# Kernel tuning notes

Hardware: AMD Instinct MI355X
Metric: run time of the kernel (lower is better)

The kernel has to match this reference:

```python
import jax, jax.numpy as jnp
import numpy as np

EMBED = 512
HEADS = 8
HEAD_DIM = EMBED // HEADS
EPS = 1e-5


def setup_inputs() -> dict:
    key = jax.random.key(0)
    ks = jax.random.split(key, 10)
    s = 1.0 / np.sqrt(EMBED)
    x = jax.random.normal(ks[0], (2, 4096, EMBED), dtype=jnp.float32)
    Wq = jax.random.uniform(ks[1], (EMBED, EMBED), jnp.float32, -s, s)
    bq = jnp.zeros((EMBED,), jnp.float32)
    Wk = jax.random.uniform(ks[2], (EMBED, EMBED), jnp.float32, -s, s)
    bk = jnp.zeros((EMBED,), jnp.float32)
    Wv = jax.random.uniform(ks[3], (EMBED, EMBED), jnp.float32, -s, s)
    bv = jnp.zeros((EMBED,), jnp.float32)
    Wo = jax.random.uniform(ks[4], (EMBED, EMBED), jnp.float32, -s, s)
    bo = jnp.zeros((EMBED,), jnp.float32)
    gamma = jnp.ones((EMBED,), jnp.float32)
    beta = jnp.zeros((EMBED,), jnp.float32)
    return {"x": x, "Wq": Wq, "bq": bq, "Wk": Wk, "bk": bk,
            "Wv": Wv, "bv": bv, "Wo": Wo, "bo": bo,
            "gamma": gamma, "beta": beta}


def reference(x, Wq, bq, Wk, bk, Wv, bv, Wo, bo, gamma, beta):
    b, n, e = x.shape
    def split_heads(t):  # [b,n,e] -> [b,h,n,d]
        return t.reshape(b, n, HEADS, HEAD_DIM).transpose(0, 2, 1, 3)
    q = split_heads(x @ Wq + bq)
    k = split_heads(x @ Wk + bk)
    v = split_heads(x @ Wv + bv)
    energy = jnp.einsum('bhqd,bhkd->bhqk', q, k) * (HEAD_DIM ** -0.5)
    attn = jax.nn.softmax(energy, axis=-1)  # dropout=0.0 (eval)
    out = jnp.einsum('bhqk,bhkd->bhqd', attn, v)
    out = out.transpose(0, 2, 1, 3).reshape(b, n, e)
    out = out @ Wo + bo
    y = x + out
    mu = jnp.mean(y, axis=-1, keepdims=True)
    var = jnp.var(y, axis=-1, keepdims=True)
    return (y - mu) * jax.lax.rsqrt(var + EPS) * gamma + beta
```

## Files before the change

### kernel.cpp

```cpp
#include <hip/hip_runtime.h>
#include <hip/hip_bf16.h>


#define ROWS 8192
#define EMB  512
#define SEQ  4096
#define HEADS 8
#define HD   64
#define QSCALE 0.18033688011112042f

typedef __attribute__((ext_vector_type(8))) short bf16x8;
typedef __attribute__((ext_vector_type(4))) short bf16x4;
typedef __attribute__((ext_vector_type(4))) float f32x4;

#define MFMA_K16(A, B, C) __builtin_amdgcn_mfma_f32_16x16x16bf16_1k(A, B, C, 0, 0, 0)

__device__ __forceinline__ float bf16_to_f(unsigned short u) {
    union { unsigned int i; float f; } v; v.i = ((unsigned int)u) << 16; return v.f;
}
__device__ __forceinline__ unsigned short f_to_bf16(float f) {
    union { __hip_bfloat16 h; unsigned short u; } v; v.h = __float2bfloat16(f); return v.u;
}
__device__ __forceinline__ unsigned int pack_bf16_trunc(float a, float b) {
    return __builtin_amdgcn_perm(__float_as_uint(b), __float_as_uint(a), 0x07060302u);
}
__device__ __forceinline__ void load_lds16(const void* g, void* l) {
    __builtin_amdgcn_global_load_lds(
        (const __attribute__((address_space(1))) void*)g,
        (__attribute__((address_space(3))) void*)l, 16, 0, 0);
}

__global__ void detect_kernel(const void* x, int* flag) {
    const unsigned short* p = (const unsigned short*)x;
    int t = threadIdx.x;
    int cnt = 0;
    for (int i = 0; i < 4; ++i) {
        unsigned short u = p[t * 4 + i];
        int e = (u >> 7) & 0xFF;
        if (e >= 140) cnt++;
    }
    for (int off = 32; off > 0; off >>= 1) cnt += __shfl_down(cnt, off, 64);
    if (t == 0) *flag = (cnt > 16) ? 1 : 0;
}

__global__ __launch_bounds__(256) void conv_x_kernel(const void* __restrict__ x,
        unsigned short* __restrict__ xb, const int* __restrict__ flag) {
    if (*flag == 0) return;
    int i = (blockIdx.x * 256 + threadIdx.x) * 4;
    float4 v = *(const float4*)((const float*)x + i);
    ushort4 u = { f_to_bf16(v.x), f_to_bf16(v.y), f_to_bf16(v.z), f_to_bf16(v.w) };
    *(ushort4*)(xb + i) = u;
}

__global__ __launch_bounds__(256) void conv_wt_kernel(
        const void* W0, const void* W1, const void* W2, const void* W3,
        unsigned short* __restrict__ Wt, const int* __restrict__ flag) {
    __shared__ float T[64][65];
    int tid = threadIdx.x;
    int kt = blockIdx.x, nt = blockIdx.y, mat = blockIdx.z;
    const void* src = (mat == 0) ? W0 : (mat == 1) ? W1 : (mat == 2) ? W2 : W3;
    int fp32 = *flag;
    for (int ii = 0; ii < 4; ++ii) {
        int idx = tid + ii * 256;
        int i = idx >> 4, j = (idx & 15) * 4;
        size_t g = (size_t)(kt * 64 + i) * 512 + nt * 64 + j;
        if (fp32) {
            float4 v = *(const float4*)((const float*)src + g);
            T[i][j] = v.x; T[i][j+1] = v.y; T[i][j+2] = v.z; T[i][j+3] = v.w;
        } else {
            ushort4 u = *(const ushort4*)((const unsigned short*)src + g);
            T[i][j] = bf16_to_f(u.x); T[i][j+1] = bf16_to_f(u.y);
            T[i][j+2] = bf16_to_f(u.z); T[i][j+3] = bf16_to_f(u.w);
        }
    }
    __syncthreads();
    for (int ii = 0; ii < 2; ++ii) {
        int idx = tid + ii * 256;
        int j = idx >> 3, ch = idx & 7;
        unsigned short pk[8];
        for (int t = 0; t < 8; ++t) pk[t] = f_to_bf16(T[ch * 8 + t][j]);
        *(bf16x8*)&Wt[(size_t)(mat * 512 + nt * 64 + j) * 512 + kt * 64 + ch * 8] = *(bf16x8*)pk;
    }
}

__global__ __launch_bounds__(256) void conv_small_kernel(
        const void* b0, const void* b1, const void* b2, const void* b3,
        const void* b4, const void* b5, float* __restrict__ dst, const int* __restrict__ flag) {
    int idx = blockIdx.x * 256 + threadIdx.x;
    int mat = idx >> 9, off = idx & 511;
    const void* src = (mat == 0) ? b0 : (mat == 1) ? b1 : (mat == 2) ? b2 :
                      (mat == 3) ? b3 : (mat == 4) ? b4 : b5;
    float v;
    if (*flag) v = ((const float*)src)[off];
    else       v = bf16_to_f(((const unsigned short*)src)[off]);
    dst[idx] = v;
}

template <typename OutT>
__global__ __launch_bounds__(256) void gemm_mfma_kernel(
        const unsigned short* __restrict__ A_conv, const unsigned short* __restrict__ A_raw,
        const int* __restrict__ flag,
        const unsigned short* __restrict__ Bt,
        const float* __restrict__ bias, OutT* __restrict__ C, int ldc, int scale_cols,
        unsigned short* __restrict__ VtOut) {
    __shared__ __align__(16) unsigned short smemg[2][2][128 * 64];
    const unsigned short* A = (*flag) ? A_conv : A_raw;
    int tid = threadIdx.x;
    int wave = tid >> 6, lane = tid & 63;
    int l15 = lane & 15, quad = lane >> 4;

    int lin = blockIdx.x + gridDim.x * blockIdx.y;
    int nwg = gridDim.x * gridDim.y;
    int bx, by;
    if (nwg & 7) { bx = blockIdx.x; by = blockIdx.y; }
    else {
        int t = (lin & 7) * (nwg >> 3) + (lin >> 3);
        bx = t % gridDim.x; by = t / gridDim.x;
    }
    int m0 = by * 128, n0 = bx * 128;
    int wm = (wave & 1) * 64, wn = (wave >> 1) * 64;

    int rt = wave * 32 + (lane >> 3);
    int ch = (lane & 7) ^ ((lane >> 3) & 7);
    const unsigned short* ag = A  + (size_t)(m0 + rt) * 512 + ch * 8;
    const unsigned short* bg = Bt + (size_t)(n0 + rt) * 512 + ch * 8;

    f32x4 acc[4][4];
    for (int i = 0; i < 4; ++i) for (int j = 0; j < 4; ++j) acc[i][j] = (f32x4){0.f,0.f,0.f,0.f};

#define GSTAGE(buf, k0) do {                                                      \
        unsigned short* Atb = &smemg[buf][0][0];                                  \
        unsigned short* Bsb = &smemg[buf][1][0];                                  \
        _Pragma("unroll")                                                         \
        for (int j = 0; j < 4; ++j) {                                             \
            load_lds16(ag + (size_t)(j * 8) * 512 + (k0), &Atb[(wave * 32 + j * 8) * 64]); \
            load_lds16(bg + (size_t)(j * 8) * 512 + (k0), &Bsb[(wave * 32 + j * 8) * 64]); \
        }                                                                         \
    } while (0)

    GSTAGE(0, 0);

    for (int s = 0; s < 8; ++s) {
        int cur = s & 1;
        asm volatile("s_waitcnt vmcnt(0)" ::: "memory");
        __builtin_amdgcn_sched_barrier(0);
        asm volatile("s_barrier" ::: "memory");
        __builtin_amdgcn_sched_barrier(0);
        if (s + 1 < 8) GSTAGE(cur ^ 1, (s + 1) * 64);

        const unsigned short* At = &smemg[cur][0][0];
        const unsigned short* Bs = &smemg[cur][1][0];
        #pragma unroll
        for (int ks = 0; ks < 2; ++ks) {
            bf16x8 a[4], b[4];
            #pragma unroll
            for (int f = 0; f < 4; ++f) {
                int pc = ((ks * 4 + quad) ^ (l15 & 7)) * 8;
                a[f] = *(const bf16x8*)&At[(wm + f * 16 + l15) * 64 + pc];
                b[f] = *(const bf16x8*)&Bs[(wn + f * 16 + l15) * 64 + pc];
            }
            #pragma unroll
            for (int fm = 0; fm < 4; ++fm)
                #pragma unroll
                for (int fn = 0; fn < 4; ++fn)
                    acc[fm][fn] = __builtin_amdgcn_mfma_f32_16x16x32_bf16(a[fm], b[fn], acc[fm][fn], 0, 0, 0);
        }
        __builtin_amdgcn_sched_barrier(0);
    }
#undef GSTAGE

    #pragma unroll
    for (int fm = 0; fm < 4; ++fm) {
        #pragma unroll
        for (int fn = 0; fn < 4; ++fn) {
            int col = n0 + wn + fn * 16 + l15;
            float bia = bias[col];
            float sc = (col < scale_cols) ? QSCALE : 1.f;
            int rowbase = m0 + wm + fm * 16 + quad * 4;
            float v0 = (acc[fm][fn][0] + bia) * sc;
            float v1 = (acc[fm][fn][1] + bia) * sc;
            float v2 = (acc[fm][fn][2] + bia) * sc;
            float v3 = (acc[fm][fn][3] + bia) * sc;
            if (VtOut && col >= 1024) {
                int hd = col - 1024;
                int bh = (rowbase >> 12) * 8 + (hd >> 6);
                int d  = hd & 63;
                ushort4 pk = { f_to_bf16(v0), f_to_bf16(v1), f_to_bf16(v2), f_to_bf16(v3) };
                *(ushort4*)&VtOut[((size_t)(bh * 64 + d)) * SEQ + (rowbase & 4095)] = pk;
            } else {
                if constexpr (sizeof(OutT) == 2) {
                    C[(size_t)(rowbase + 0) * ldc + col] = (OutT)f_to_bf16(v0);
                    C[(size_t)(rowbase + 1) * ldc + col] = (OutT)f_to_bf16(v1);
                    C[(size_t)(rowbase + 2) * ldc + col] = (OutT)f_to_bf16(v2);
                    C[(size_t)(rowbase + 3) * ldc + col] = (OutT)f_to_bf16(v3);
                } else {
                    C[(size_t)(rowbase + 0) * ldc + col] = v0;
                    C[(size_t)(rowbase + 1) * ldc + col] = v1;
                    C[(size_t)(rowbase + 2) * ldc + col] = v2;
                    C[(size_t)(rowbase + 3) * ldc + col] = v3;
                }
            }
        }
    }
}

__global__ __launch_bounds__(256, 4) void attn_kernel(
        const unsigned short* __restrict__ QKV, const unsigned short* __restrict__ Vt,
        unsigned short* __restrict__ Ab) {
    __shared__ __align__(16) unsigned char smem[32768];
    float* Ored = (float*)smem;
    float* Lred = (float*)(smem + 16384);

    int tid = threadIdx.x;
    int wave = tid >> 6, lane = tid & 63;
    int l15 = lane & 15, quad = lane >> 4;
    int qh = wave >> 1, kh = wave & 1;
    int lin = blockIdx.x;
    int xcd = lin & 7, slot = lin >> 3;
    int grp = xcd + 8 * (slot >> 6);
    int qt = slot & 63;
    int h = grp & 7, b = grp >> 3;
    int bh = b * HEADS + h;
    size_t qrow0 = (size_t)b * SEQ + qt * 64;

    bf16x8 aq[2][2];
    #pragma unroll
    for (int t = 0; t < 2; ++t) {
        const unsigned short* qp = &QKV[(qrow0 + qh * 32 + t * 16 + l15) * 1536 + h * 64];
        aq[t][0] = *(const bf16x8*)&qp[quad * 8];
        aq[t][1] = *(const bf16x8*)&qp[32 + quad * 8];
    }
    f32x4 o[2][4];
    #pragma unroll
    for (int t = 0; t < 2; ++t)
        #pragma unroll
        for (int db = 0; db < 4; ++db) o[t][db] = (f32x4){0.f, 0.f, 0.f, 0.f};
    float lp[2] = {0.f, 0.f};

    int r8 = lane >> 3;
    int kch = (lane & 7) ^ (r8 & 7);
    const unsigned short* kg = &QKV[((size_t)b * SEQ + r8) * 1536 + 512 + h * 64 + kch * 8];
    const unsigned short* vg = &Vt[((size_t)bh * 64 + wave * 16 + r8) * SEQ + kch * 8];

#define STAGE(buf, kt2) do {                                                          \
        unsigned short* Ksb = (unsigned short*)(smem + (buf) * 8192);                 \
        unsigned short* Vsb = (unsigned short*)(smem + 16384 + (buf) * 8192);         \
        load_lds16(kg + (size_t)((kt2) * 64 + wave * 16) * 1536,                      \
                   &Ksb[(wave * 16) * 64]);                                           \
        load_lds16(kg + (size_t)((kt2) * 64 + wave * 16 + 8) * 1536,                  \
                   &Ksb[(wave * 16 + 8) * 64]);                                       \
        load_lds16(vg + (size_t)((kt2) * 64), &Vsb[(wave * 16) * 64]);                \
        load_lds16(vg + (size_t)((kt2) * 64) + (size_t)8 * SEQ,                       \
                   &Vsb[(wave * 16 + 8) * 64]);                                       \
    } while (0)

    STAGE(0, 0);

    for (int kt = 0; kt < SEQ / 64; ++kt) {
        int cur = kt & 1;
        asm volatile("s_waitcnt vmcnt(0)" ::: "memory");
        __builtin_amdgcn_sched_barrier(0);
        asm volatile("s_barrier" ::: "memory");
        __builtin_amdgcn_sched_barrier(0);
        if (kt + 1 < SEQ / 64) STAGE(cur ^ 1, kt + 1);

        const unsigned short* Ksc = (const unsigned short*)(smem + cur * 8192);
        const unsigned short* Vsc = (const unsigned short*)(smem + 16384 + cur * 8192);
        #pragma unroll
        for (int nb = 0; nb < 2; ++nb) {
            int kc = kh * 32 + nb * 16;
            int krow = kc + l15;
            int key = krow & 7;
            bf16x8 kA0 = *(const bf16x8*)&Ksc[krow * 64 + (quad ^ key) * 8];
            bf16x8 kA1 = *(const bf16x8*)&Ksc[krow * 64 + ((4 + quad) ^ key) * 8];
            bf16x4 bv[4];
            #pragma unroll
            for (int db = 0; db < 4; ++db) {
                int d = db * 16 + l15;
                int c16 = (kc >> 3) + (quad >> 1);
                int sub = (quad & 1) * 4;
                bv[db] = *(const bf16x4*)&Vsc[d * 64 + ((c16 ^ (d & 7)) * 8) + sub];
            }
            #pragma unroll
            for (int t = 0; t < 2; ++t) {
                f32x4 sv = {0.f, 0.f, 0.f, 0.f};
                __builtin_amdgcn_s_setprio(1);
                sv = __builtin_amdgcn_mfma_f32_16x16x32_bf16(kA0, aq[t][0], sv, 0, 0, 0);
                sv = __builtin_amdgcn_mfma_f32_16x16x32_bf16(kA1, aq[t][1], sv, 0, 0, 0);
                __builtin_amdgcn_s_setprio(0);
                float p0 = __builtin_amdgcn_exp2f(sv[0]);
                float p1 = __builtin_amdgcn_exp2f(sv[1]);
                float p2 = __builtin_amdgcn_exp2f(sv[2]);
                float p3 = __builtin_amdgcn_exp2f(sv[3]);
                lp[t] += (p0 + p1) + (p2 + p3);
                union { unsigned int u[2]; bf16x4 v; } ap;
                ap.u[0] = pack_bf16_trunc(p0, p1);
                ap.u[1] = pack_bf16_trunc(p2, p3);
                __builtin_amdgcn_s_setprio(1);
                #pragma unroll
                for (int db = 0; db < 4; ++db)
                    o[t][db] = MFMA_K16(ap.v, bv[db], o[t][db]);
                __builtin_amdgcn_s_setprio(0);
            }
        }
        __builtin_amdgcn_sched_barrier(0);
    }
#undef STAGE

    __syncthreads();
    #pragma unroll
    for (int t = 0; t < 2; ++t) {
        float v = lp[t];
        v += __shfl_xor(v, 16, 64);
        v += __shfl_xor(v, 32, 64);
        if (quad == 0) Lred[(wave * 2 + t) * 16 + l15] = v;
    }
    __syncthreads();
    float* myO = Ored + wave * (16 * 64);
    #pragma unroll
    for (int t = 0; t < 2; ++t) {
        #pragma unroll
        for (int db = 0; db < 4; ++db)
            #pragma unroll
            for (int r = 0; r < 4; ++r)
                myO[(quad * 4 + r) * 64 + db * 16 + l15] = o[t][db][r];
        __syncthreads();
        {
            int q_l = tid >> 3;
            int dg = tid & 7;
            int qh2 = q_l >> 4, qq = q_l & 15;
            const float* r0 = Ored + (qh2 * 2 + 0) * (16 * 64) + qq * 64 + dg * 8;
            const float* r1 = Ored + (qh2 * 2 + 1) * (16 * 64) + qq * 64 + dg * 8;
            float4 a0 = *(const float4*)&r0[0];
            float4 a1 = *(const float4*)&r0[4];
            float4 c0 = *(const float4*)&r1[0];
            float4 c1 = *(const float4*)&r1[4];
            float lt = Lred[((qh2 * 2 + 0) * 2 + t) * 16 + qq] +
                       Lred[((qh2 * 2 + 1) * 2 + t) * 16 + qq];
            float inv = 1.f / lt;
            size_t row = qrow0 + qh2 * 32 + t * 16 + qq;
            unsigned short* dst = &Ab[row * EMB + h * 64 + dg * 8];
            ushort4 lo = { f_to_bf16((a0.x + c0.x) * inv), f_to_bf16((a0.y + c0.y) * inv),
                           f_to_bf16((a0.z + c0.z) * inv), f_to_bf16((a0.w + c0.w) * inv) };
            ushort4 hi = { f_to_bf16((a1.x + c1.x) * inv), f_to_bf16((a1.y + c1.y) * inv),
                           f_to_bf16((a1.z + c1.z) * inv), f_to_bf16((a1.w + c1.w) * inv) };
            *(ushort4*)&dst[0] = lo;
            *(ushort4*)&dst[4] = hi;
        }
        __syncthreads();
    }
}

__global__ __launch_bounds__(256) void ln_kernel(
        const float* __restrict__ xf, const unsigned short* __restrict__ xraw,
        const unsigned short* __restrict__ P,
        const float* __restrict__ gamma, const float* __restrict__ beta,
        void* __restrict__ out, const int* __restrict__ flag) {
    int row = blockIdx.x * 4 + (threadIdx.x >> 6);
    int t = threadIdx.x & 63;
    int fp32 = *flag;
    float v[8];
    float s = 0.f, ss = 0.f;
    const unsigned short* pp = &P[(size_t)row * EMB + t * 8];
    ushort4 p0 = *(const ushort4*)&pp[0];
    ushort4 p1 = *(const ushort4*)&pp[4];
    float pv[8] = { bf16_to_f(p0.x), bf16_to_f(p0.y), bf16_to_f(p0.z), bf16_to_f(p0.w),
                    bf16_to_f(p1.x), bf16_to_f(p1.y), bf16_to_f(p1.z), bf16_to_f(p1.w) };
    if (fp32) {
        const float* xp = &xf[(size_t)row * EMB + t * 8];
        for (int i = 0; i < 8; i += 4) {
            float4 x4 = *(const float4*)&xp[i];
            v[i] = x4.x + pv[i]; v[i+1] = x4.y + pv[i+1];
            v[i+2] = x4.z + pv[i+2]; v[i+3] = x4.w + pv[i+3];
        }
    } else {
        const unsigned short* xp = &xraw[(size_t)row * EMB + t * 8];
        ushort4 x0 = *(const ushort4*)&xp[0];
        ushort4 x1 = *(const ushort4*)&xp[4];
        v[0] = bf16_to_f(x0.x) + pv[0]; v[1] = bf16_to_f(x0.y) + pv[1];
        v[2] = bf16_to_f(x0.z) + pv[2]; v[3] = bf16_to_f(x0.w) + pv[3];
        v[4] = bf16_to_f(x1.x) + pv[4]; v[5] = bf16_to_f(x1.y) + pv[5];
        v[6] = bf16_to_f(x1.z) + pv[6]; v[7] = bf16_to_f(x1.w) + pv[7];
    }
    for (int i = 0; i < 8; ++i) { s += v[i]; ss += v[i] * v[i]; }
    for (int off = 32; off > 0; off >>= 1) {
        s  += __shfl_xor(s, off, 64);
        ss += __shfl_xor(ss, off, 64);
    }
    float mu = s * (1.f / 512.f);
    float var = ss * (1.f / 512.f) - mu * mu;
    float rs = rsqrtf(var + 1e-5f);
    for (int i = 0; i < 8; ++i) {
        int col = t * 8 + i;
        float y = (v[i] - mu) * rs * gamma[col] + beta[col];
        if (fp32) ((float*)out)[(size_t)row * EMB + col] = y;
        else      ((__hip_bfloat16*)out)[(size_t)row * EMB + col] = __float2bfloat16(y);
    }
}

extern "C" void kernel_launch(void* const* d_in, const int* in_sizes, int n_in,
                              void* d_out, int out_size, void* d_ws, size_t ws_size,
                              hipStream_t stream) {
    char* ws = (char*)d_ws;
    int* flag = (int*)ws;
    char* p = ws + 256;
    float* bias_all = (float*)p;       p += 6 * 512 * 4;
    unsigned short* Wt   = (unsigned short*)p; p += (size_t)2048 * 512 * 2;
    unsigned short* QKVb = (unsigned short*)p; p += (size_t)ROWS * 1536 * 2;
    unsigned short* Vt   = (unsigned short*)p; p += (size_t)16 * HD * SEQ * 2;
    unsigned short* xb = (unsigned short*)p;
    unsigned short* Ab = (unsigned short*)p;   p += (size_t)ROWS * EMB * 2;
    unsigned short* Pb = (unsigned short*)p;   p += (size_t)ROWS * EMB * 2;

    detect_kernel<<<1, 64, 0, stream>>>(d_in[0], flag);

    conv_x_kernel<<<ROWS * EMB / 1024, 256, 0, stream>>>(d_in[0], xb, flag);
    conv_wt_kernel<<<dim3(8, 8, 4), 256, 0, stream>>>(d_in[1], d_in[3], d_in[5], d_in[7], Wt, flag);
    conv_small_kernel<<<12, 256, 0, stream>>>(d_in[2], d_in[4], d_in[6], d_in[8], d_in[9], d_in[10],
                                              bias_all, flag);

    gemm_mfma_kernel<unsigned short><<<dim3(12, 64), 256, 0, stream>>>(
        xb, (const unsigned short*)d_in[0], flag, Wt, bias_all, QKVb, 1536, 512, Vt);

    attn_kernel<<<dim3(1024), 256, 0, stream>>>(QKVb, Vt, Ab);

    gemm_mfma_kernel<unsigned short><<<dim3(4, 64), 256, 0, stream>>>(
        Ab, Ab, flag, Wt + (size_t)1536 * 512, bias_all + 1536, Pb, 512, 0,
        (unsigned short*)nullptr);

    ln_kernel<<<ROWS / 4, 256, 0, stream>>>((const float*)d_in[0],
                                            (const unsigned short*)d_in[0], Pb,
                                            bias_all + 4 * 512, bias_all + 5 * 512, d_out, flag);
}
```

Baseline: 238.0 us.

## Use K=32 MFMA for PV via permuted key staging; merge prep kernels

```diff
diff --git a/kernel.cpp b/kernel.cpp
--- a/kernel.cpp
+++ b/kernel.cpp
@@ -13,8 +13,6 @@
 typedef __attribute__((ext_vector_type(4))) short bf16x4;
 typedef __attribute__((ext_vector_type(4))) float f32x4;
 
-#define MFMA_K16(A, B, C) __builtin_amdgcn_mfma_f32_16x16x16bf16_1k(A, B, C, 0, 0, 0)
-
 __device__ __forceinline__ float bf16_to_f(unsigned short u) {
     union { unsigned int i; float f; } v; v.i = ((unsigned int)u) << 16; return v.f;
 }
@@ -30,81 +28,82 @@
         (__attribute__((address_space(3))) void*)l, 16, 0, 0);
 }
 
-__global__ void detect_kernel(const void* x, int* flag) {
+__device__ __forceinline__ int detect_fp32(const void* x) {
     const unsigned short* p = (const unsigned short*)x;
-    int t = threadIdx.x;
+    int t = threadIdx.x & 63;
     int cnt = 0;
+    #pragma unroll
     for (int i = 0; i < 4; ++i) {
         unsigned short u = p[t * 4 + i];
         int e = (u >> 7) & 0xFF;
-        if (e >= 140) cnt++;
-    }
-    for (int off = 32; off > 0; off >>= 1) cnt += __shfl_down(cnt, off, 64);
-    if (t == 0) *flag = (cnt > 16) ? 1 : 0;
-}
-
-__global__ __launch_bounds__(256) void conv_x_kernel(const void* __restrict__ x,
-        unsigned short* __restrict__ xb, const int* __restrict__ flag) {
-    if (*flag == 0) return;
-    int i = (blockIdx.x * 256 + threadIdx.x) * 4;
-    float4 v = *(const float4*)((const float*)x + i);
-    ushort4 u = { f_to_bf16(v.x), f_to_bf16(v.y), f_to_bf16(v.z), f_to_bf16(v.w) };
-    *(ushort4*)(xb + i) = u;
-}
-
-__global__ __launch_bounds__(256) void conv_wt_kernel(
+        cnt += (e >= 140) ? 1 : 0;
+    }
+    #pragma unroll
+    for (int off = 32; off > 0; off >>= 1) cnt += __shfl_xor(cnt, off, 64);
+    return cnt > 16;
+}
+
+__global__ __launch_bounds__(256) void prep_kernel(
+        const void* __restrict__ x, unsigned short* __restrict__ xb,
         const void* W0, const void* W1, const void* W2, const void* W3,
-        unsigned short* __restrict__ Wt, const int* __restrict__ flag) {
-    __shared__ float T[64][65];
+        unsigned short* __restrict__ Wt,
+        const void* b0, const void* b1, const void* b2, const void* b3,
+        const void* b4, const void* b5, float* __restrict__ bias_all) {
+    int fp32 = detect_fp32(x);
+    int bid = blockIdx.x;
     int tid = threadIdx.x;
-    int kt = blockIdx.x, nt = blockIdx.y, mat = blockIdx.z;
-    const void* src = (mat == 0) ? W0 : (mat == 1) ? W1 : (mat == 2) ? W2 : W3;
-    int fp32 = *flag;
-    for (int ii = 0; ii < 4; ++ii) {
-        int idx = tid + ii * 256;
-        int i = idx >> 4, j = (idx & 15) * 4;
-        size_t g = (size_t)(kt * 64 + i) * 512 + nt * 64 + j;
-        if (fp32) {
-            float4 v = *(const float4*)((const float*)src + g);
-            T[i][j] = v.x; T[i][j+1] = v.y; T[i][j+2] = v.z; T[i][j+3] = v.w;
-        } else {
-            ushort4 u = *(const ushort4*)((const unsigned short*)src + g);
-            T[i][j] = bf16_to_f(u.x); T[i][j+1] = bf16_to_f(u.y);
-            T[i][j+2] = bf16_to_f(u.z); T[i][j+3] = bf16_to_f(u.w);
-        }
-    }
-    __syncthreads();
-    for (int ii = 0; ii < 2; ++ii) {
-        int idx = tid + ii * 256;
-        int j = idx >> 3, ch = idx & 7;
-        unsigned short pk[8];
-        for (int t = 0; t < 8; ++t) pk[t] = f_to_bf16(T[ch * 8 + t][j]);
-        *(bf16x8*)&Wt[(size_t)(mat * 512 + nt * 64 + j) * 512 + kt * 64 + ch * 8] = *(bf16x8*)pk;
-    }
-}
-
-__global__ __launch_bounds__(256) void conv_small_kernel(
-        const void* b0, const void* b1, const void* b2, const void* b3,
-        const void* b4, const void* b5, float* __restrict__ dst, const int* __restrict__ flag) {
-    int idx = blockIdx.x * 256 + threadIdx.x;
-    int mat = idx >> 9, off = idx & 511;
-    const void* src = (mat == 0) ? b0 : (mat == 1) ? b1 : (mat == 2) ? b2 :
-                      (mat == 3) ? b3 : (mat == 4) ? b4 : b5;
-    float v;
-    if (*flag) v = ((const float*)src)[off];
-    else       v = bf16_to_f(((const unsigned short*)src)[off]);
-    dst[idx] = v;
+    if (bid < 4096) {
+        if (!fp32) return;
+        int i = (bid * 256 + tid) * 4;
+        float4 v = *(const float4*)((const float*)x + i);
+        ushort4 u = { f_to_bf16(v.x), f_to_bf16(v.y), f_to_bf16(v.z), f_to_bf16(v.w) };
+        *(ushort4*)(xb + i) = u;
+    } else if (bid < 4352) {
+        __shared__ float T[64][65];
+        int idx0 = bid - 4096;
+        int kt = idx0 & 7, nt = (idx0 >> 3) & 7, mat = idx0 >> 6;
+        const void* src = (mat == 0) ? W0 : (mat == 1) ? W1 : (mat == 2) ? W2 : W3;
+        for (int ii = 0; ii < 4; ++ii) {
+            int idx = tid + ii * 256;
+            int i = idx >> 4, j = (idx & 15) * 4;
+            size_t g = (size_t)(kt * 64 + i) * 512 + nt * 64 + j;
+            if (fp32) {
+                float4 v = *(const float4*)((const float*)src + g);
+                T[i][j] = v.x; T[i][j+1] = v.y; T[i][j+2] = v.z; T[i][j+3] = v.w;
+            } else {
+                ushort4 u = *(const ushort4*)((const unsigned short*)src + g);
+                T[i][j] = bf16_to_f(u.x); T[i][j+1] = bf16_to_f(u.y);
+                T[i][j+2] = bf16_to_f(u.z); T[i][j+3] = bf16_to_f(u.w);
+            }
+        }
+        __syncthreads();
+        for (int ii = 0; ii < 2; ++ii) {
+            int idx = tid + ii * 256;
+            int j = idx >> 3, ch = idx & 7;
+            unsigned short pk[8];
+            for (int t = 0; t < 8; ++t) pk[t] = f_to_bf16(T[ch * 8 + t][j]);
+            *(bf16x8*)&Wt[(size_t)(mat * 512 + nt * 64 + j) * 512 + kt * 64 + ch * 8] = *(bf16x8*)pk;
+        }
+    } else {
+        int idx = (bid - 4352) * 256 + tid;
+        int mat = idx >> 9, off = idx & 511;
+        const void* src = (mat == 0) ? b0 : (mat == 1) ? b1 : (mat == 2) ? b2 :
+                          (mat == 3) ? b3 : (mat == 4) ? b4 : b5;
+        float v;
+        if (fp32) v = ((const float*)src)[off];
+        else      v = bf16_to_f(((const unsigned short*)src)[off]);
+        bias_all[idx] = v;
+    }
 }
 
 template <typename OutT>
 __global__ __launch_bounds__(256) void gemm_mfma_kernel(
         const unsigned short* __restrict__ A_conv, const unsigned short* __restrict__ A_raw,
-        const int* __restrict__ flag,
         const unsigned short* __restrict__ Bt,
         const float* __restrict__ bias, OutT* __restrict__ C, int ldc, int scale_cols,
         unsigned short* __restrict__ VtOut) {
     __shared__ __align__(16) unsigned short smemg[2][2][128 * 64];
-    const unsigned short* A = (*flag) ? A_conv : A_raw;
+    const unsigned short* A = detect_fp32(A_raw) ? A_conv : A_raw;
     int tid = threadIdx.x;
     int wave = tid >> 6, lane = tid & 63;
     int l15 = lane & 15, quad = lane >> 4;
@@ -239,16 +238,19 @@
 
     int r8 = lane >> 3;
     int kch = (lane & 7) ^ (r8 & 7);
-    const unsigned short* kg = &QKV[((size_t)b * SEQ + r8) * 1536 + 512 + h * 64 + kch * 8];
+    int r0 = wave * 16 + r8;
+    int r1 = wave * 16 + 8 + r8;
+    int p0r = (r0 & 32) | (((r0 >> 2) & 3) << 3) | (((r0 >> 4) & 1) << 2) | (r0 & 3);
+    int p1r = (r1 & 32) | (((r1 >> 2) & 3) << 3) | (((r1 >> 4) & 1) << 2) | (r1 & 3);
+    const unsigned short* kg0 = &QKV[((size_t)b * SEQ + p0r) * 1536 + 512 + h * 64 + kch * 8];
+    const unsigned short* kg1 = &QKV[((size_t)b * SEQ + p1r) * 1536 + 512 + h * 64 + kch * 8];
     const unsigned short* vg = &Vt[((size_t)bh * 64 + wave * 16 + r8) * SEQ + kch * 8];
 
 #define STAGE(buf, kt2) do {                                                          \
         unsigned short* Ksb = (unsigned short*)(smem + (buf) * 8192);                 \
         unsigned short* Vsb = (unsigned short*)(smem + 16384 + (buf) * 8192);         \
-        load_lds16(kg + (size_t)((kt2) * 64 + wave * 16) * 1536,                      \
-                   &Ksb[(wave * 16) * 64]);                                           \
-        load_lds16(kg + (size_t)((kt2) * 64 + wave * 16 + 8) * 1536,                  \
-                   &Ksb[(wave * 16 + 8) * 64]);                                       \
+        load_lds16(kg0 + (size_t)((kt2) * 64) * 1536, &Ksb[(wave * 16) * 64]);        \
+        load_lds16(kg1 + (size_t)((kt2) * 64) * 1536, &Ksb[(wave * 16 + 8) * 64]);    \
         load_lds16(vg + (size_t)((kt2) * 64), &Vsb[(wave * 16) * 64]);                \
         load_lds16(vg + (size_t)((kt2) * 64) + (size_t)8 * SEQ,                       \
                    &Vsb[(wave * 16 + 8) * 64]);                                       \
@@ -266,42 +268,50 @@
 
         const unsigned short* Ksc = (const unsigned short*)(smem + cur * 8192);
         const unsigned short* Vsc = (const unsigned short*)(smem + 16384 + cur * 8192);
+
+        bf16x8 kA[2][2];
         #pragma unroll
         for (int nb = 0; nb < 2; ++nb) {
-            int kc = kh * 32 + nb * 16;
-            int krow = kc + l15;
+            int krow = kh * 32 + nb * 16 + l15;
             int key = krow & 7;
-            bf16x8 kA0 = *(const bf16x8*)&Ksc[krow * 64 + (quad ^ key) * 8];
-            bf16x8 kA1 = *(const bf16x8*)&Ksc[krow * 64 + ((4 + quad) ^ key) * 8];
-            bf16x4 bv[4];
+            kA[nb][0] = *(const bf16x8*)&Ksc[krow * 64 + (quad ^ key) * 8];
+            kA[nb][1] = *(const bf16x8*)&Ksc[krow * 64 + ((4 + quad) ^ key) * 8];
+        }
+        bf16x8 bv8[4];
+        #pragma unroll
+        for (int db = 0; db < 4; ++db) {
+            int d = db * 16 + l15;
+            bv8[db] = *(const bf16x8*)&Vsc[d * 64 + (((kh * 4 + quad) ^ (d & 7))) * 8];
+        }
+        #pragma unroll
+        for (int t = 0; t < 2; ++t) {
+            f32x4 sv0 = {0.f, 0.f, 0.f, 0.f};
+            f32x4 sv1 = {0.f, 0.f, 0.f, 0.f};
+            __builtin_amdgcn_s_setprio(1);
+            sv0 = __builtin_amdgcn_mfma_f32_16x16x32_bf16(kA[0][0], aq[t][0], sv0, 0, 0, 0);
+            sv0 = __builtin_amdgcn_mfma_f32_16x16x32_bf16(kA[0][1], aq[t][1], sv0, 0, 0, 0);
+            sv1 = __builtin_amdgcn_mfma_f32_16x16x32_bf16(kA[1][0], aq[t][0], sv1, 0, 0, 0);
+            sv1 = __builtin_amdgcn_mfma_f32_16x16x32_bf16(kA[1][1], aq[t][1], sv1, 0, 0, 0);
+            __builtin_amdgcn_s_setprio(0);
+            float p0 = __builtin_amdgcn_exp2f(sv0[0]);
+            float p1 = __builtin_amdgcn_exp2f(sv0[1]);
+            float p2 = __builtin_amdgcn_exp2f(sv0[2]);
+            float p3 = __builtin_amdgcn_exp2f(sv0[3]);
+            float p4 = __builtin_amdgcn_exp2f(sv1[0]);
+            float p5 = __builtin_amdgcn_exp2f(sv1[1]);
+            float p6 = __builtin_amdgcn_exp2f(sv1[2]);
+            float p7 = __builtin_amdgcn_exp2f(sv1[3]);
+            lp[t] += ((p0 + p1) + (p2 + p3)) + ((p4 + p5) + (p6 + p7));
+            union { unsigned int u[4]; bf16x8 v; } ap;
+            ap.u[0] = pack_bf16_trunc(p0, p1);
+            ap.u[1] = pack_bf16_trunc(p2, p3);
+            ap.u[2] = pack_bf16_trunc(p4, p5);
+            ap.u[3] = pack_bf16_trunc(p6, p7);
+            __builtin_amdgcn_s_setprio(1);
             #pragma unroll
-            for (int db = 0; db < 4; ++db) {
-                int d = db * 16 + l15;
-                int c16 = (kc >> 3) + (quad >> 1);
-                int sub = (quad & 1) * 4;
-                bv[db] = *(const bf16x4*)&Vsc[d * 64 + ((c16 ^ (d & 7)) * 8) + sub];
-            }
-            #pragma unroll
-            for (int t = 0; t < 2; ++t) {
-                f32x4 sv = {0.f, 0.f, 0.f, 0.f};
-                __builtin_amdgcn_s_setprio(1);
-                sv = __builtin_amdgcn_mfma_f32_16x16x32_bf16(kA0, aq[t][0], sv, 0, 0, 0);
-                sv = __builtin_amdgcn_mfma_f32_16x16x32_bf16(kA1, aq[t][1], sv, 0, 0, 0);
-                __builtin_amdgcn_s_setprio(0);
-                float p0 = __builtin_amdgcn_exp2f(sv[0]);
-                float p1 = __builtin_amdgcn_exp2f(sv[1]);
-                float p2 = __builtin_amdgcn_exp2f(sv[2]);
-                float p3 = __builtin_amdgcn_exp2f(sv[3]);
-                lp[t] += (p0 + p1) + (p2 + p3);
-                union { unsigned int u[2]; bf16x4 v; } ap;
-                ap.u[0] = pack_bf16_trunc(p0, p1);
-                ap.u[1] = pack_bf16_trunc(p2, p3);
-                __builtin_amdgcn_s_setprio(1);
-                #pragma unroll
-                for (int db = 0; db < 4; ++db)
-                    o[t][db] = MFMA_K16(ap.v, bv[db], o[t][db]);
-                __builtin_amdgcn_s_setprio(0);
-            }
+            for (int db = 0; db < 4; ++db)
+                o[t][db] = __builtin_amdgcn_mfma_f32_16x16x32_bf16(ap.v, bv8[db], o[t][db], 0, 0, 0);
+            __builtin_amdgcn_s_setprio(0);
         }
         __builtin_amdgcn_sched_barrier(0);
     }
@@ -329,12 +339,12 @@
             int q_l = tid >> 3;
             int dg = tid & 7;
             int qh2 = q_l >> 4, qq = q_l & 15;
-            const float* r0 = Ored + (qh2 * 2 + 0) * (16 * 64) + qq * 64 + dg * 8;
-            const float* r1 = Ored + (qh2 * 2 + 1) * (16 * 64) + qq * 64 + dg * 8;
-            float4 a0 = *(const float4*)&r0[0];
-            float4 a1 = *(const float4*)&r0[4];
-            float4 c0 = *(const float4*)&r1[0];
-            float4 c1 = *(const float4*)&r1[4];
+            const float* r0p = Ored + (qh2 * 2 + 0) * (16 * 64) + qq * 64 + dg * 8;
+            const float* r1p = Ored + (qh2 * 2 + 1) * (16 * 64) + qq * 64 + dg * 8;
+            float4 a0 = *(const float4*)&r0p[0];
+            float4 a1 = *(const float4*)&r0p[4];
+            float4 c0 = *(const float4*)&r1p[0];
+            float4 c1 = *(const float4*)&r1p[4];
             float lt = Lred[((qh2 * 2 + 0) * 2 + t) * 16 + qq] +
                        Lred[((qh2 * 2 + 1) * 2 + t) * 16 + qq];
             float inv = 1.f / lt;
@@ -355,10 +365,10 @@
         const float* __restrict__ xf, const unsigned short* __restrict__ xraw,
         const unsigned short* __restrict__ P,
         const float* __restrict__ gamma, const float* __restrict__ beta,
-        void* __restrict__ out, const int* __restrict__ flag) {
+        void* __restrict__ out) {
+    int fp32 = detect_fp32(xraw);
     int row = blockIdx.x * 4 + (threadIdx.x >> 6);
     int t = threadIdx.x & 63;
-    int fp32 = *flag;
     float v[8];
     float s = 0.f, ss = 0.f;
     const unsigned short* pp = &P[(size_t)row * EMB + t * 8];
@@ -402,7 +412,6 @@
                               void* d_out, int out_size, void* d_ws, size_t ws_size,
                               hipStream_t stream) {
     char* ws = (char*)d_ws;
-    int* flag = (int*)ws;
     char* p = ws + 256;
     float* bias_all = (float*)p;       p += 6 * 512 * 4;
     unsigned short* Wt   = (unsigned short*)p; p += (size_t)2048 * 512 * 2;
@@ -412,23 +421,20 @@
     unsigned short* Ab = (unsigned short*)p;   p += (size_t)ROWS * EMB * 2;
     unsigned short* Pb = (unsigned short*)p;   p += (size_t)ROWS * EMB * 2;
 
-    detect_kernel<<<1, 64, 0, stream>>>(d_in[0], flag);
-
-    conv_x_kernel<<<ROWS * EMB / 1024, 256, 0, stream>>>(d_in[0], xb, flag);
-    conv_wt_kernel<<<dim3(8, 8, 4), 256, 0, stream>>>(d_in[1], d_in[3], d_in[5], d_in[7], Wt, flag);
-    conv_small_kernel<<<12, 256, 0, stream>>>(d_in[2], d_in[4], d_in[6], d_in[8], d_in[9], d_in[10],
-                                              bias_all, flag);
+    prep_kernel<<<4364, 256, 0, stream>>>(d_in[0], xb,
+        d_in[1], d_in[3], d_in[5], d_in[7], Wt,
+        d_in[2], d_in[4], d_in[6], d_in[8], d_in[9], d_in[10], bias_all);
 
     gemm_mfma_kernel<unsigned short><<<dim3(12, 64), 256, 0, stream>>>(
-        xb, (const unsigned short*)d_in[0], flag, Wt, bias_all, QKVb, 1536, 512, Vt);
+        xb, (const unsigned short*)d_in[0], Wt, bias_all, QKVb, 1536, 512, Vt);
 
     attn_kernel<<<dim3(1024), 256, 0, stream>>>(QKVb, Vt, Ab);
 
     gemm_mfma_kernel<unsigned short><<<dim3(4, 64), 256, 0, stream>>>(
-        Ab, Ab, flag, Wt + (size_t)1536 * 512, bias_all + 1536, Pb, 512, 0,
+        Ab, Ab, Wt + (size_t)1536 * 512, bias_all + 1536, Pb, 512, 0,
         (unsigned short*)nullptr);
 
     ln_kernel<<<ROWS / 4, 256, 0, stream>>>((const float*)d_in[0],
                                             (const unsigned short*)d_in[0], Pb,
-                                            bias_all + 4 * 512, bias_all + 5 * 512, d_out, flag);
-}
+                                            bias_all + 4 * 512, bias_all + 5 * 512, d_out);
+}
```

After: 220.5 us. 7.3% less time.
